# Optimization experiments

Measured on AMD Instinct MI355X. Metric: run time of the kernel, lower is better.

## Reference

```python
import jax, jax.numpy as jnp
import numpy as np

B, T, D = 4, 2048, 1024
H = 16
HD = D // H          # per-head dim (dk/heads = dv/heads = 64)
FF = 2048            # FFN default hidden_dim
EPS = 1e-5


def _ln(x, g, b):
    mu = jnp.mean(x, -1, keepdims=True)
    var = jnp.mean((x - mu) ** 2, -1, keepdims=True)
    return (x - mu) * jax.lax.rsqrt(var + EPS) * g + b


def setup_inputs() -> dict:
    key = jax.random.key(0)
    ks = jax.random.split(key, 12)
    s_in = 1.0 / np.sqrt(D)
    s_ff = 1.0 / np.sqrt(FF)
    return {
        "x": jax.random.normal(ks[0], (B, T, D), jnp.float32),
        # per-head projections stacked: [H, D, HD]
        "Wq": jax.random.uniform(ks[1], (H, D, HD), jnp.float32, -s_in, s_in),
        "bq": jnp.zeros((H, HD), jnp.float32),
        "Wk": jax.random.uniform(ks[2], (H, D, HD), jnp.float32, -s_in, s_in),
        "bk": jnp.zeros((H, HD), jnp.float32),
        "Wv": jax.random.uniform(ks[3], (H, D, HD), jnp.float32, -s_in, s_in),
        "bv": jnp.zeros((H, HD), jnp.float32),
        "Wo": jax.random.uniform(ks[4], (D, D), jnp.float32, -s_in, s_in),
        "bo": jnp.zeros((D,), jnp.float32),
        "ln1_g": jnp.ones((D,), jnp.float32),
        "ln1_b": jnp.zeros((D,), jnp.float32),
        "W1": jax.random.uniform(ks[5], (D, FF), jnp.float32, -s_in, s_in),
        "b1": jnp.zeros((FF,), jnp.float32),
        "W2": jax.random.uniform(ks[6], (FF, D), jnp.float32, -s_ff, s_ff),
        "b2": jnp.zeros((D,), jnp.float32),
        "ln2_g": jnp.ones((D,), jnp.float32),
        "ln2_b": jnp.zeros((D,), jnp.float32),
    }


def reference(x, Wq, bq, Wk, bk, Wv, bv, Wo, bo, ln1_g, ln1_b, W1, b1, W2, b2, ln2_g, ln2_b):
    # QKV projections (per-head Linear loop vectorized over H): [B,H,T,HD]
    q = jnp.einsum("btd,hdk->bhtk", x, Wq) + bq[:, None, :]
    k = jnp.einsum("btd,hdk->bhtk", x, Wk) + bk[:, None, :]
    v = jnp.einsum("btd,hdk->bhtk", x, Wv) + bv[:, None, :]
    # scaled dot-product attention; scale uses per-head dk = HD
    scores = jnp.einsum("bhtk,bhsk->bhts", q, k) / jnp.sqrt(jnp.float32(HD))
    weights = jax.nn.softmax(scores, axis=-1)
    ctx = jnp.einsum("bhts,bhsk->bhtk", weights, v)        # [B,H,T,HD]
    # concat heads along last dim (head order preserved) then output proj
    ctx = ctx.transpose(0, 2, 1, 3).reshape(B, T, D)
    c = ctx @ Wo + bo
    # residual + LayerNorm
    x = _ln(x + c, ln1_g, ln1_b)
    # FFN: Linear -> ReLU -> Linear
    y = jax.nn.relu(x @ W1 + b1) @ W2 + b2
    return _ln(x + y, ln2_g, ln2_b)
```

## Files before the change

### kernel.cpp

```cpp
#include <hip/hip_runtime.h>
#include <hip/hip_bf16.h>

#define BB 4
#define TT 2048
#define DD 1024
#define HH 16
#define HD 64
#define FF 2048
#define QSCL 0.1803368801111204f

typedef unsigned short u16;
typedef __bf16 bf16x8 __attribute__((ext_vector_type(8)));
typedef float f32x4 __attribute__((ext_vector_type(4)));
typedef float f32x16 __attribute__((ext_vector_type(16)));
typedef unsigned short u16x8 __attribute__((ext_vector_type(8)));
typedef unsigned short u16x4 __attribute__((ext_vector_type(4)));
typedef unsigned int u32x4 __attribute__((ext_vector_type(4)));

__device__ __forceinline__ u16 f2bf(float f) {
    return __builtin_bit_cast(u16, (__bf16)f);
}
__device__ __forceinline__ float bf2f(u16 u) {
    return __builtin_bit_cast(float, (unsigned)u << 16);
}
__device__ __forceinline__ float exp2fast(float x) {
    float r;
    asm("v_exp_f32 %0, %1" : "=v"(r) : "v"(x));
    return r;
}
__device__ __forceinline__ void gload16(const void* g, void* l) {
    __builtin_amdgcn_global_load_lds((const __attribute__((address_space(1))) void*)g,
                                     (__attribute__((address_space(3))) void*)l, 16, 0, 0);
}

__global__ __launch_bounds__(256) void convert_x(const float* __restrict__ in, u16* __restrict__ out, int n8) {
    int i = blockIdx.x * 256 + threadIdx.x;
    if (i >= n8) return;
    const float4* p = (const float4*)in + (size_t)i * 2;
    float4 a = p[0], b = p[1];
    u16x8 o;
    o[0] = f2bf(a.x); o[1] = f2bf(a.y); o[2] = f2bf(a.z); o[3] = f2bf(a.w);
    o[4] = f2bf(b.x); o[5] = f2bf(b.y); o[6] = f2bf(b.z); o[7] = f2bf(b.w);
    ((u16x8*)out)[i] = o;
}

__global__ __launch_bounds__(256) void transpose_conv(const float* __restrict__ in, u16* __restrict__ out, int R, int C) {
    __shared__ float tile[32][33];
    const int c0 = blockIdx.x * 32, r0 = blockIdx.y * 32;
    const int tx = threadIdx.x & 31, ty = threadIdx.x >> 5;
#pragma unroll
    for (int j = 0; j < 4; ++j) tile[ty + j * 8][tx] = in[(size_t)(r0 + ty + j * 8) * C + c0 + tx];
    __syncthreads();
#pragma unroll
    for (int j = 0; j < 4; ++j) out[(size_t)(c0 + ty + j * 8) * R + r0 + tx] = f2bf(tile[tx][ty + j * 8]);
}

__global__ __launch_bounds__(256) void qkv_transpose(const float* __restrict__ Wq, const float* __restrict__ Wk,
                                                     const float* __restrict__ Wv, u16* __restrict__ out) {
    __shared__ float tile[32][33];
    const int z = blockIdx.z, w = z >> 4, h = z & 15;
    const float* in = (w == 0 ? Wq : (w == 1 ? Wk : Wv)) + (size_t)h * (DD * HD);
    u16* op = out + (size_t)(w * 1024 + h * 64) * DD;
    const int c0 = blockIdx.x * 32, r0 = blockIdx.y * 32;
    const int tx = threadIdx.x & 31, ty = threadIdx.x >> 5;
#pragma unroll
    for (int j = 0; j < 4; ++j) tile[ty + j * 8][tx] = in[(size_t)(r0 + ty + j * 8) * HD + c0 + tx];
    __syncthreads();
#pragma unroll
    for (int j = 0; j < 4; ++j) op[(size_t)(c0 + ty + j * 8) * DD + r0 + tx] = f2bf(tile[tx][ty + j * 8]);
}

__global__ __launch_bounds__(256) void pack_bias(const float* __restrict__ bq, const float* __restrict__ bk,
                                                 const float* __restrict__ bv, float* __restrict__ out) {
    int i = blockIdx.x * 256 + threadIdx.x;
    if (i < 3072) {
        const float* s = i < 1024 ? bq : (i < 2048 ? bk : bv);
        out[i] = s[i & 1023];
    }
}

template <int EPI, int BN>
__global__ __launch_bounds__(512, 2) void gemm256(const u16* __restrict__ A, const u16* __restrict__ Bt,
                                                  const float* __restrict__ bias, const void* __restrict__ res,
                                                  void* __restrict__ outp, void* __restrict__ outp2,
                                                  int M, int N, int K) {
    constexpr int NFR = BN / 64;
    constexpr int NB = BN / 64;
    __shared__ __align__(16) u16 sA[2][256 * 64];
    __shared__ __align__(16) u16 sB[2][BN * 64];
    const int t = threadIdx.x;
    const int lane = t & 63, wv = t >> 6;
    const int wm = (wv >> 2) * 128, wn = (wv & 3) * (BN / 4);
    const int lq = lane & 15, lk8 = (lane >> 4) * 8;
    const int lr = lane >> 3, ch = lane & 7;
    const int colel = (ch ^ lr) << 3;
    const int nwg = gridDim.x * gridDim.y;
    const int bid = blockIdx.y * gridDim.x + blockIdx.x;
    const int swz = (bid & 7) * (nwg >> 3) + (bid >> 3);
    const int m0 = (swz / gridDim.x) * 256, n0 = (swz % gridDim.x) * BN;

    const u16* Ag = A + ((size_t)m0 + lr) * K + colel;
    const u16* Bg = Bt + ((size_t)n0 + lr) * K + colel;

#define STAGE_A(buf, slot, k0)                                                           \
    do {                                                                                 \
        _Pragma("unroll") for (int j = 0; j < 2; ++j) {                                  \
            int row0 = (slot)*64 + j * 128 + wv * 8;                                     \
            gload16(Ag + (size_t)row0 * K + (k0), (char*)sA + (buf)*32768 + row0 * 128); \
        }                                                                                \
    } while (0)
#define STAGE_B(buf, k0)                                                                          \
    do {                                                                                          \
        _Pragma("unroll") for (int j = 0; j < NB; ++j) {                                          \
            int row0 = j * 64 + wv * 8;                                                           \
            gload16(Bg + (size_t)row0 * K + (k0), (char*)sB + (buf) * (BN * 128) + row0 * 128);   \
        }                                                                                         \
    } while (0)

    f32x4 acc[8][NFR];
#pragma unroll
    for (int i = 0; i < 8; ++i)
#pragma unroll
        for (int j = 0; j < NFR; ++j) acc[i][j] = (f32x4){0.f, 0.f, 0.f, 0.f};

    STAGE_A(0, 0, 0);
    STAGE_B(0, 0);
    STAGE_A(0, 1, 0);
    asm volatile("s_waitcnt vmcnt(0)" ::: "memory");
    __builtin_amdgcn_s_barrier();
    __builtin_amdgcn_sched_barrier(0);

    const int nk = K / 64;
    for (int kt = 0; kt < nk; ++kt) {
        const int cur = kt & 1, nxt = cur ^ 1;
        const int k1 = (kt + 1) * 64;
        const bool pf = (kt + 1 < nk);
        const char* sAc = (const char*)sA + cur * 32768;
        const char* sBc = (const char*)sB + cur * (BN * 128);
        bf16x8 a[4][2], b[NFR][2];

#pragma unroll
        for (int mf = 0; mf < 4; ++mf)
#pragma unroll
            for (int kk = 0; kk < 2; ++kk) {
                int row = wm + mf * 16 + lq;
                a[mf][kk] = *(const bf16x8*)(sAc + ((row * 128 + kk * 64 + lk8 * 2) ^ ((row & 7) << 4)));
            }
#pragma unroll
        for (int nf = 0; nf < NFR; ++nf)
#pragma unroll
            for (int kk = 0; kk < 2; ++kk) {
                int row = wn + nf * 16 + lq;
                b[nf][kk] = *(const bf16x8*)(sBc + ((row * 128 + kk * 64 + lk8 * 2) ^ ((row & 7) << 4)));
            }
        if (pf) {
            STAGE_A(nxt, 0, k1);
            STAGE_B(nxt, k1);
        }
        asm volatile("s_waitcnt lgkmcnt(0)" ::: "memory");
        __builtin_amdgcn_sched_barrier(0);
        __builtin_amdgcn_s_setprio(1);
#pragma unroll
        for (int mf = 0; mf < 4; ++mf)
#pragma unroll
            for (int nf = 0; nf < NFR; ++nf) {
                acc[mf][nf] = __builtin_amdgcn_mfma_f32_16x16x32_bf16(a[mf][0], b[nf][0], acc[mf][nf], 0, 0, 0);
                acc[mf][nf] = __builtin_amdgcn_mfma_f32_16x16x32_bf16(a[mf][1], b[nf][1], acc[mf][nf], 0, 0, 0);
            }
        __builtin_amdgcn_s_setprio(0);
        __builtin_amdgcn_sched_barrier(0);
        if (pf) {
            if (BN == 256)
                asm volatile("s_waitcnt vmcnt(6)" ::: "memory");
            else
                asm volatile("s_waitcnt vmcnt(4)" ::: "memory");
        } else {
            asm volatile("s_waitcnt vmcnt(0)" ::: "memory");
        }
        __builtin_amdgcn_s_barrier();
        __builtin_amdgcn_sched_barrier(0);

#pragma unroll
        for (int mf = 0; mf < 4; ++mf)
#pragma unroll
            for (int kk = 0; kk < 2; ++kk) {
                int row = wm + 64 + mf * 16 + lq;
                a[mf][kk] = *(const bf16x8*)(sAc + ((row * 128 + kk * 64 + lk8 * 2) ^ ((row & 7) << 4)));
            }
        if (pf) STAGE_A(nxt, 1, k1);
        asm volatile("s_waitcnt lgkmcnt(0)" ::: "memory");
        __builtin_amdgcn_sched_barrier(0);
        __builtin_amdgcn_s_setprio(1);
#pragma unroll
        for (int mf = 0; mf < 4; ++mf)
#pragma unroll
            for (int nf = 0; nf < NFR; ++nf) {
                acc[mf + 4][nf] = __builtin_amdgcn_mfma_f32_16x16x32_bf16(a[mf][0], b[nf][0], acc[mf + 4][nf], 0, 0, 0);
                acc[mf + 4][nf] = __builtin_amdgcn_mfma_f32_16x16x32_bf16(a[mf][1], b[nf][1], acc[mf + 4][nf], 0, 0, 0);
            }
        __builtin_amdgcn_s_setprio(0);
        __builtin_amdgcn_sched_barrier(0);
        if (pf)
            asm volatile("s_waitcnt vmcnt(2)" ::: "memory");
        __builtin_amdgcn_s_barrier();
        __builtin_amdgcn_sched_barrier(0);
    }

    const int rbase = (lane >> 4) * 4;
#pragma unroll
    for (int mf = 0; mf < 8; ++mf) {
#pragma unroll
        for (int nf = 0; nf < NFR; ++nf) {
            int gn = n0 + wn + nf * 16 + lq;
            float bv = bias[gn];
            if (EPI == 0) {
                int which = gn >> 10, hh = (gn >> 6) & 15, hd = gn & 63;
                int gm0 = m0 + wm + mf * 16 + rbase;
                int b2 = gm0 >> 11, tt2 = gm0 & 2047;
                if (which == 2) {
                    u16x4 pk;
#pragma unroll
                    for (int r = 0; r < 4; ++r) pk[r] = f2bf(acc[mf][nf][r] + bv);
                    *(u16x4*)((u16*)outp2 + ((size_t)(b2 * HH + hh) * HD + hd) * TT + tt2) = pk;
                } else {
                    float scl = (which == 0) ? QSCL : 1.f;
                    size_t off0 = (size_t)which * ((size_t)BB * HH * TT * HD) +
                                  ((size_t)(b2 * HH + hh) * TT + tt2) * HD + hd;
#pragma unroll
                    for (int r = 0; r < 4; ++r)
                        ((u16*)outp)[off0 + (size_t)r * HD] = f2bf((acc[mf][nf][r] + bv) * scl);
                }
            } else {
#pragma unroll
                for (int r = 0; r < 4; ++r) {
                    int gm = m0 + wm + mf * 16 + rbase + r;
                    size_t idx = (size_t)gm * N + gn;
                    float val = acc[mf][nf][r] + bv;
                    if (EPI == 2) {
                        ((u16*)outp)[idx] = f2bf(val > 0.f ? val : 0.f);
                    } else if (EPI == 1) {
                        ((u16*)outp)[idx] = f2bf(val + ((const float*)res)[idx]);
                    } else {
                        ((u16*)outp)[idx] = f2bf(val + bf2f(((const u16*)res)[idx]));
                    }
                }
            }
        }
    }
#undef STAGE_A
#undef STAGE_B
}

__global__ __launch_bounds__(512) void attn_kernel(const u16* __restrict__ qk, const u16* __restrict__ vt,
                                                   u16* __restrict__ ctx) {
    const int t = threadIdx.x, wv = t >> 6, lane = t & 63;
    const int l31 = lane & 31, hi = lane >> 5;
    const int lr = lane >> 3, ch = lane & 7;
    const int colel = (ch ^ lr) << 3;
    const int bid = blockIdx.y * 8 + blockIdx.x;
    const int swz = (bid & 7) * 64 + (bid >> 3);
    const int qt = swz & 7, bh = swz >> 3;
    const size_t WSTR = (size_t)BB * HH * TT * HD;
    const u16* qp = qk + (size_t)bh * TT * HD;
    const u16* kp = qp + WSTR;
    const u16* vtp = vt + (size_t)bh * HD * TT;
    const int qr = qt * 256 + wv * 32;

    __shared__ __align__(16) u16 sK[2][64 * 64];
    __shared__ __align__(16) u16 sVt[2][64 * 64];

    const u16* kbase = kp + (size_t)(wv * 8 + lr) * HD + colel;
    const u16* vbase = vtp + (size_t)(wv * 8 + lr) * TT + colel;
    char* dK = (char*)sK + wv * 1024;
    char* dV = (char*)sVt + wv * 1024;

#define ATTN_STAGE(bufi, kb)                                        \
    do {                                                            \
        gload16(kbase + (size_t)(kb)*HD, dK + (bufi)*8192);         \
        gload16(vbase + (kb), dV + (bufi)*8192);                    \
    } while (0)

    bf16x8 qf[4];
#pragma unroll
    for (int c = 0; c < 4; ++c)
        qf[c] = *(const bf16x8*)(qp + (size_t)(qr + l31) * HD + c * 16 + 8 * hi);

    int off[2][4];
#pragma unroll
    for (int half = 0; half < 2; ++half)
#pragma unroll
        for (int c = 0; c < 4; ++c) {
            int row = half * 32 + l31;
            off[half][c] = row * 128 + (((c * 16 + 8 * hi) * 2) ^ ((row & 7) << 4));
        }

    f32x16 psv = (f32x16)0.f;
    f32x16 oacc[2];
    oacc[0] = (f32x16)0.f;
    oacc[1] = (f32x16)0.f;

    ATTN_STAGE(0, 0);

    const int NT = TT / 64;
    for (int kt = 0; kt < NT; ++kt) {
        const int cur = kt & 1;
        if (kt + 1 < NT) {
            ATTN_STAGE(cur ^ 1, (kt + 1) * 64);
            asm volatile("s_waitcnt vmcnt(2)" ::: "memory");
        } else {
            asm volatile("s_waitcnt vmcnt(0)" ::: "memory");
        }
        __builtin_amdgcn_s_barrier();
        __builtin_amdgcn_sched_barrier(0);

        const char* sKc = (const char*)sK + cur * 8192;
        const char* sVc = (const char*)sVt + cur * 8192;

        f32x16 sacc[2];
        sacc[0] = (f32x16)0.f;
        sacc[1] = (f32x16)0.f;
#pragma unroll
        for (int kb2 = 0; kb2 < 2; ++kb2)
#pragma unroll
            for (int c = 0; c < 4; ++c) {
                bf16x8 kf = *(const bf16x8*)(sKc + off[kb2][c]);
                sacc[kb2] = __builtin_amdgcn_mfma_f32_32x32x16_bf16(kf, qf[c], sacc[kb2], 0, 0, 0);
            }

#pragma unroll
        for (int kb2 = 0; kb2 < 2; ++kb2) {
#pragma unroll
            for (int i = 0; i < 16; ++i) sacc[kb2][i] = exp2fast(sacc[kb2][i]);
            psv += sacc[kb2];
        }

        bf16x8 pfrag[4];
#pragma unroll
        for (int kb2 = 0; kb2 < 2; ++kb2)
#pragma unroll
            for (int c2 = 0; c2 < 2; ++c2) {
                const int base = c2 * 8;
                unsigned a0, a1, b0, b1;
                asm("v_cvt_pk_bf16_f32 %0, %1, %2" : "=v"(a0) : "v"(sacc[kb2][base + 0]), "v"(sacc[kb2][base + 1]));
                asm("v_cvt_pk_bf16_f32 %0, %1, %2" : "=v"(a1) : "v"(sacc[kb2][base + 2]), "v"(sacc[kb2][base + 3]));
                asm("v_cvt_pk_bf16_f32 %0, %1, %2" : "=v"(b0) : "v"(sacc[kb2][base + 4]), "v"(sacc[kb2][base + 5]));
                asm("v_cvt_pk_bf16_f32 %0, %1, %2" : "=v"(b1) : "v"(sacc[kb2][base + 6]), "v"(sacc[kb2][base + 7]));
                asm("v_permlane32_swap_b32 %0, %1" : "+v"(a0), "+v"(b0));
                asm("v_permlane32_swap_b32 %0, %1" : "+v"(a1), "+v"(b1));
                u32x4 w = {a0, a1, b0, b1};
                pfrag[kb2 * 2 + c2] = __builtin_bit_cast(bf16x8, w);
            }

#pragma unroll
        for (int db = 0; db < 2; ++db)
#pragma unroll
            for (int kc = 0; kc < 4; ++kc) {
                bf16x8 vf = *(const bf16x8*)(sVc + off[db][kc]);
                oacc[db] = __builtin_amdgcn_mfma_f32_32x32x16_bf16(vf, pfrag[kc], oacc[db], 0, 0, 0);
            }

        __builtin_amdgcn_sched_barrier(0);
        __builtin_amdgcn_s_barrier();
    }

    float ls = 0.f;
#pragma unroll
    for (int i = 0; i < 16; ++i) ls += psv[i];
    ls += __shfl_xor(ls, 32);
    const float inv = 1.f / ls;

    const int b = bh >> 4, h = bh & 15;
    u16* orow = ctx + ((size_t)b * TT + (qr + l31)) * DD + h * HD;
#pragma unroll
    for (int db = 0; db < 2; ++db)
#pragma unroll
        for (int rq = 0; rq < 4; ++rq) {
            u16x4 ov;
#pragma unroll
            for (int j = 0; j < 4; ++j) ov[j] = f2bf(oacc[db][rq * 4 + j] * inv);
            *(u16x4*)(orow + db * 32 + rq * 8 + 4 * hi) = ov;
        }
#undef ATTN_STAGE
}

template <bool OUTF32>
__global__ __launch_bounds__(256) void ln_kernel(const u16* __restrict__ y, const float* __restrict__ g,
                                                 const float* __restrict__ b, float* __restrict__ of,
                                                 u16* __restrict__ ob) {
    const int row = blockIdx.x, t = threadIdx.x;
    const u16x4 raw = *(const u16x4*)(y + (size_t)row * DD + t * 4);
    float v0 = bf2f(raw[0]), v1 = bf2f(raw[1]), v2 = bf2f(raw[2]), v3 = bf2f(raw[3]);
    float s = v0 + v1 + v2 + v3;
    float q = v0 * v0 + v1 * v1 + v2 * v2 + v3 * v3;
#pragma unroll
    for (int m = 1; m < 64; m <<= 1) {
        s += __shfl_xor(s, m);
        q += __shfl_xor(q, m);
    }
    __shared__ float red[8];
    const int wv = t >> 6, ln = t & 63;
    if (ln == 0) {
        red[wv] = s;
        red[4 + wv] = q;
    }
    __syncthreads();
    s = red[0] + red[1] + red[2] + red[3];
    q = red[4] + red[5] + red[6] + red[7];
    const float mu = s * (1.f / DD);
    const float var = q * (1.f / DD) - mu * mu;
    const float rstd = rsqrtf(var + 1e-5f);
    const float4 gg = ((const float4*)g)[t];
    const float4 bb = ((const float4*)b)[t];
    float o0 = (v0 - mu) * rstd * gg.x + bb.x;
    float o1 = (v1 - mu) * rstd * gg.y + bb.y;
    float o2 = (v2 - mu) * rstd * gg.z + bb.z;
    float o3 = (v3 - mu) * rstd * gg.w + bb.w;
    if (OUTF32) {
        ((float4*)(of + (size_t)row * DD))[t] = (float4){o0, o1, o2, o3};
    } else {
        u16x4 u;
        u[0] = f2bf(o0); u[1] = f2bf(o1); u[2] = f2bf(o2); u[3] = f2bf(o3);
        *(u16x4*)(ob + (size_t)row * DD + t * 4) = u;
    }
}

extern "C" void kernel_launch(void* const* d_in, const int* in_sizes, int n_in,
                              void* d_out, int out_size, void* d_ws, size_t ws_size,
                              hipStream_t stream) {
    const float* x   = (const float*)d_in[0];
    const float* Wq  = (const float*)d_in[1];
    const float* bq  = (const float*)d_in[2];
    const float* Wk  = (const float*)d_in[3];
    const float* bk  = (const float*)d_in[4];
    const float* Wv  = (const float*)d_in[5];
    const float* bv  = (const float*)d_in[6];
    const float* Wo  = (const float*)d_in[7];
    const float* bo  = (const float*)d_in[8];
    const float* g1  = (const float*)d_in[9];
    const float* be1 = (const float*)d_in[10];
    const float* W1  = (const float*)d_in[11];
    const float* b1  = (const float*)d_in[12];
    const float* W2  = (const float*)d_in[13];
    const float* b2  = (const float*)d_in[14];
    const float* g2  = (const float*)d_in[15];
    const float* be2 = (const float*)d_in[16];
    float* out = (float*)d_out;

    char* ws = (char*)d_ws;
    u16*   xb    = (u16*)(ws + 0);
    u16*   wqkvt = (u16*)(ws + 16777216);
    u16*   wot   = (u16*)(ws + 23068672);
    u16*   w1t   = (u16*)(ws + 25165824);
    u16*   w2t   = (u16*)(ws + 29360128);
    float* bqkv  = (float*)(ws + 33554432);
    u16*   qkb   = (u16*)(ws + 33566720);
    u16*   vtb   = qkb + (size_t)2 * BB * HH * TT * HD;
    u16*   y1b   = (u16*)(ws + 83898368);
    u16*   x1b   = (u16*)(ws + 100675584);
    u16*   ctx   = xb;
    u16*   hbuf  = qkb;
    u16*   y2b   = y1b;

    const int M = BB * TT;

    convert_x<<<dim3((M * DD / 8 + 255) / 256), 256, 0, stream>>>(x, xb, M * DD / 8);
    qkv_transpose<<<dim3(2, 32, 48), 256, 0, stream>>>(Wq, Wk, Wv, wqkvt);
    transpose_conv<<<dim3(32, 32), 256, 0, stream>>>(Wo, wot, DD, DD);
    transpose_conv<<<dim3(64, 32), 256, 0, stream>>>(W1, w1t, DD, FF);
    transpose_conv<<<dim3(32, 64), 256, 0, stream>>>(W2, w2t, FF, DD);
    pack_bias<<<dim3(12), 256, 0, stream>>>(bq, bk, bv, bqkv);

    gemm256<0, 256><<<dim3(3 * DD / 256, M / 256), 512, 0, stream>>>(xb, wqkvt, bqkv, nullptr, qkb, vtb, M, 3 * DD, DD);
    attn_kernel<<<dim3(8, BB * HH), 512, 0, stream>>>(qkb, vtb, ctx);
    gemm256<1, 128><<<dim3(DD / 128, M / 256), 512, 0, stream>>>(ctx, wot, bo, x, y1b, nullptr, M, DD, DD);
    ln_kernel<false><<<dim3(M), 256, 0, stream>>>(y1b, g1, be1, nullptr, x1b);
    gemm256<2, 256><<<dim3(FF / 256, M / 256), 512, 0, stream>>>(x1b, w1t, b1, nullptr, hbuf, nullptr, M, FF, DD);
    gemm256<3, 128><<<dim3(DD / 128, M / 256), 512, 0, stream>>>(hbuf, w2t, b2, x1b, y2b, nullptr, M, DD, FF);
    ln_kernel<true><<<dim3(M), 256, 0, stream>>>(y2b, g2, be2, out, nullptr);
}
```

Baseline: 285.0 us.

## Load V fragments directly from global into registers in attention loop

Attention no longer stages V^T tiles through shared memory. Each wave issues eight dwordx4 global loads per key tile straight into MFMA operand registers, with the waitcnt logic reworked so the QK/softmax phase overlaps those loads. The per-tile row sums are also folded into a scalar accumulator instead of a 16-wide vector. This cuts LDS traffic and halves the shared allocation, but every one of the 8 waves now reads the same V tile separately from global/L2, and the load latency is exposed inside the loop without double buffering.

```diff
diff --git a/kernel.cpp b/kernel.cpp
--- a/kernel.cpp
+++ b/kernel.cpp
@@ -264,21 +264,16 @@
     const u16* qp = qk + (size_t)bh * TT * HD;
     const u16* kp = qp + WSTR;
     const u16* vtp = vt + (size_t)bh * HD * TT;
+    const unsigned long long vts = (unsigned long long)vtp;
     const int qr = qt * 256 + wv * 32;
 
     __shared__ __align__(16) u16 sK[2][64 * 64];
-    __shared__ __align__(16) u16 sVt[2][64 * 64];
 
     const u16* kbase = kp + (size_t)(wv * 8 + lr) * HD + colel;
-    const u16* vbase = vtp + (size_t)(wv * 8 + lr) * TT + colel;
     char* dK = (char*)sK + wv * 1024;
-    char* dV = (char*)sVt + wv * 1024;
-
-#define ATTN_STAGE(bufi, kb)                                        \
-    do {                                                            \
-        gload16(kbase + (size_t)(kb)*HD, dK + (bufi)*8192);         \
-        gload16(vbase + (kb), dV + (bufi)*8192);                    \
-    } while (0)
+
+    const unsigned vb0 = (unsigned)l31 * (TT * 2) + hi * 16;
+    const unsigned vb1 = vb0 + 32 * TT * 2;
 
     bf16x8 qf[4];
 #pragma unroll
@@ -294,78 +289,86 @@
             off[half][c] = row * 128 + (((c * 16 + 8 * hi) * 2) ^ ((row & 7) << 4));
         }
 
-    f32x16 psv = (f32x16)0.f;
+    float ls = 0.f;
     f32x16 oacc[2];
     oacc[0] = (f32x16)0.f;
     oacc[1] = (f32x16)0.f;
 
-    ATTN_STAGE(0, 0);
+    gload16(kbase, dK);
 
     const int NT = TT / 64;
     for (int kt = 0; kt < NT; ++kt) {
         const int cur = kt & 1;
+        const unsigned voff0 = vb0 + (unsigned)kt * 128;
+        const unsigned voff1 = vb1 + (unsigned)kt * 128;
+        bf16x8 vreg[2][4];
+        asm volatile("global_load_dwordx4 %0, %1, %2 offset:0"  : "=v"(vreg[0][0]) : "v"(voff0), "s"(vts));
+        asm volatile("global_load_dwordx4 %0, %1, %2 offset:32" : "=v"(vreg[0][1]) : "v"(voff0), "s"(vts));
+        asm volatile("global_load_dwordx4 %0, %1, %2 offset:64" : "=v"(vreg[0][2]) : "v"(voff0), "s"(vts));
+        asm volatile("global_load_dwordx4 %0, %1, %2 offset:96" : "=v"(vreg[0][3]) : "v"(voff0), "s"(vts));
+        asm volatile("global_load_dwordx4 %0, %1, %2 offset:0"  : "=v"(vreg[1][0]) : "v"(voff1), "s"(vts));
+        asm volatile("global_load_dwordx4 %0, %1, %2 offset:32" : "=v"(vreg[1][1]) : "v"(voff1), "s"(vts));
+        asm volatile("global_load_dwordx4 %0, %1, %2 offset:64" : "=v"(vreg[1][2]) : "v"(voff1), "s"(vts));
+        asm volatile("global_load_dwordx4 %0, %1, %2 offset:96" : "=v"(vreg[1][3]) : "v"(voff1), "s"(vts));
+        __builtin_amdgcn_sched_barrier(0);
         if (kt + 1 < NT) {
-            ATTN_STAGE(cur ^ 1, (kt + 1) * 64);
-            asm volatile("s_waitcnt vmcnt(2)" ::: "memory");
+            gload16(kbase + (size_t)((kt + 1) * 64) * HD, dK + (cur ^ 1) * 8192);
+            asm volatile("s_waitcnt vmcnt(9)" ::: "memory");
         } else {
-            asm volatile("s_waitcnt vmcnt(0)" ::: "memory");
+            asm volatile("s_waitcnt vmcnt(8)" ::: "memory");
         }
         __builtin_amdgcn_s_barrier();
         __builtin_amdgcn_sched_barrier(0);
 
         const char* sKc = (const char*)sK + cur * 8192;
-        const char* sVc = (const char*)sVt + cur * 8192;
-
-        f32x16 sacc[2];
-        sacc[0] = (f32x16)0.f;
-        sacc[1] = (f32x16)0.f;
-#pragma unroll
-        for (int kb2 = 0; kb2 < 2; ++kb2)
+
+        bf16x8 pfrag[4];
+        float ts = 0.f;
+#pragma unroll
+        for (int kb2 = 0; kb2 < 2; ++kb2) {
+            f32x16 sacc = (f32x16)0.f;
 #pragma unroll
             for (int c = 0; c < 4; ++c) {
                 bf16x8 kf = *(const bf16x8*)(sKc + off[kb2][c]);
-                sacc[kb2] = __builtin_amdgcn_mfma_f32_32x32x16_bf16(kf, qf[c], sacc[kb2], 0, 0, 0);
-            }
-
-#pragma unroll
-        for (int kb2 = 0; kb2 < 2; ++kb2) {
-#pragma unroll
-            for (int i = 0; i < 16; ++i) sacc[kb2][i] = exp2fast(sacc[kb2][i]);
-            psv += sacc[kb2];
-        }
-
-        bf16x8 pfrag[4];
-#pragma unroll
-        for (int kb2 = 0; kb2 < 2; ++kb2)
+                sacc = __builtin_amdgcn_mfma_f32_32x32x16_bf16(kf, qf[c], sacc, 0, 0, 0);
+            }
+#pragma unroll
+            for (int i = 0; i < 16; ++i) {
+                sacc[i] = exp2fast(sacc[i]);
+                ts += sacc[i];
+            }
 #pragma unroll
             for (int c2 = 0; c2 < 2; ++c2) {
                 const int base = c2 * 8;
                 unsigned a0, a1, b0, b1;
-                asm("v_cvt_pk_bf16_f32 %0, %1, %2" : "=v"(a0) : "v"(sacc[kb2][base + 0]), "v"(sacc[kb2][base + 1]));
-                asm("v_cvt_pk_bf16_f32 %0, %1, %2" : "=v"(a1) : "v"(sacc[kb2][base + 2]), "v"(sacc[kb2][base + 3]));
-                asm("v_cvt_pk_bf16_f32 %0, %1, %2" : "=v"(b0) : "v"(sacc[kb2][base + 4]), "v"(sacc[kb2][base + 5]));
-                asm("v_cvt_pk_bf16_f32 %0, %1, %2" : "=v"(b1) : "v"(sacc[kb2][base + 6]), "v"(sacc[kb2][base + 7]));
+                asm("v_cvt_pk_bf16_f32 %0, %1, %2" : "=v"(a0) : "v"(sacc[base + 0]), "v"(sacc[base + 1]));
+                asm("v_cvt_pk_bf16_f32 %0, %1, %2" : "=v"(a1) : "v"(sacc[base + 2]), "v"(sacc[base + 3]));
+                asm("v_cvt_pk_bf16_f32 %0, %1, %2" : "=v"(b0) : "v"(sacc[base + 4]), "v"(sacc[base + 5]));
+                asm("v_cvt_pk_bf16_f32 %0, %1, %2" : "=v"(b1) : "v"(sacc[base + 6]), "v"(sacc[base + 7]));
                 asm("v_permlane32_swap_b32 %0, %1" : "+v"(a0), "+v"(b0));
                 asm("v_permlane32_swap_b32 %0, %1" : "+v"(a1), "+v"(b1));
                 u32x4 w = {a0, a1, b0, b1};
                 pfrag[kb2 * 2 + c2] = __builtin_bit_cast(bf16x8, w);
             }
+        }
+        ls += ts;
+
+        if (kt + 1 < NT)
+            asm volatile("s_waitcnt vmcnt(1)" ::: "memory");
+        else
+            asm volatile("s_waitcnt vmcnt(0)" ::: "memory");
+        __builtin_amdgcn_sched_barrier(0);
 
 #pragma unroll
         for (int db = 0; db < 2; ++db)
 #pragma unroll
-            for (int kc = 0; kc < 4; ++kc) {
-                bf16x8 vf = *(const bf16x8*)(sVc + off[db][kc]);
-                oacc[db] = __builtin_amdgcn_mfma_f32_32x32x16_bf16(vf, pfrag[kc], oacc[db], 0, 0, 0);
-            }
+            for (int kc = 0; kc < 4; ++kc)
+                oacc[db] = __builtin_amdgcn_mfma_f32_32x32x16_bf16(vreg[db][kc], pfrag[kc], oacc[db], 0, 0, 0);
 
         __builtin_amdgcn_sched_barrier(0);
         __builtin_amdgcn_s_barrier();
     }
 
-    float ls = 0.f;
-#pragma unroll
-    for (int i = 0; i < 16; ++i) ls += psv[i];
     ls += __shfl_xor(ls, 32);
     const float inv = 1.f / ls;
 
@@ -380,7 +383,6 @@
             for (int j = 0; j < 4; ++j) ov[j] = f2bf(oacc[db][rq * 4 + j] * inv);
             *(u16x4*)(orow + db * 32 + rq * 8 + 4 * hi) = ov;
         }
-#undef ATTN_STAGE
 }
 
 template <bool OUTF32>
```

Measured after the change: 366.4 us. 28.5% more time.
